# Performance work log

Measured on AMD Instinct MI355X. Metric: run time of the kernel, lower is better.

## Reference

```python
import jax, jax.numpy as jnp
import numpy as np

NUM_HEADING_BIN = 12
NUM_SIZE_CLUSTER = 8
DELTA_NORM_W = 0.01
CENTER_W = 0.5
B, N = 4096, 2048


def huber(err, delta=1.0):
    a = jnp.abs(err)
    q = jnp.minimum(a, delta)
    return jnp.mean(0.5 * q * q + delta * (a - q))


def box3d_corners(centers, headings, sizes):
    # centers (B,3), headings (B,), sizes (B,3) -> (B,8,3)
    l, w, h = sizes[:, 0:1], sizes[:, 1:2], sizes[:, 2:3]
    sx = jnp.asarray([1, 1, -1, -1, 1, 1, -1, -1], dtype=sizes.dtype)
    sy = jnp.asarray([1, -1, -1, 1, 1, -1, -1, 1], dtype=sizes.dtype)
    sz = jnp.asarray([1, 1, 1, 1, -1, -1, -1, -1], dtype=sizes.dtype)
    corners = jnp.stack([0.5 * l * sx, 0.5 * w * sy, 0.5 * h * sz], axis=1)  # (B,3,8)
    c, s = jnp.cos(headings), jnp.sin(headings)
    z, o = jnp.zeros_like(c), jnp.ones_like(c)
    R = jnp.stack([jnp.stack([c, -s, z], -1),
                   jnp.stack([s, c, z], -1),
                   jnp.stack([z, z, o], -1)], axis=1)  # (B,3,3)
    out = jnp.einsum('bij,bjk->bik', R, corners) + centers[:, :, None]
    return jnp.transpose(out, (0, 2, 1))  # (B,8,3)


def setup_inputs() -> dict:
    key = jax.random.key(0)
    ks = jax.random.split(key, 9)
    return {
        'mask_xyz_mean': jax.random.normal(ks[0], (B, 3), jnp.float32),
        'point_cloud': jax.random.normal(ks[1], (B, 3, N), jnp.float32),
        'x_delta': jax.random.normal(ks[2], (B, 3, N), jnp.float32),
        'center_label': jax.random.normal(ks[3], (B, 3), jnp.float32),
        'size_residual_label': jax.random.normal(ks[4], (B, 3), jnp.float32),
        'heading_residual_label': jax.random.normal(ks[5], (B,), jnp.float32),
        'mean_sizes': jax.random.uniform(ks[6], (NUM_SIZE_CLUSTER, 3), jnp.float32, 0.5, 2.5),
        'size_class_label': jax.random.randint(ks[7], (B,), 0, NUM_SIZE_CLUSTER, jnp.int32),
        'heading_class_label': jax.random.randint(ks[8], (B,), 0, NUM_HEADING_BIN, jnp.int32),
    }


def reference(mask_xyz_mean, point_cloud, x_delta, center_label,
              size_residual_label, heading_residual_label, mean_sizes,
              size_class_label, heading_class_label):
    eps = 0.0  # faithful: original has no eps
    # center loss
    center_dist = jnp.linalg.norm(mask_xyz_mean - center_label, axis=1)
    center_loss = CENTER_W * huber(center_dist)

    # label assembly (onehot-sum == gather)
    size_label = mean_sizes[size_class_label] + size_residual_label  # (B,3)
    bin_centers = jnp.arange(0, np.pi, np.pi / NUM_HEADING_BIN, dtype=jnp.float32)
    heading_label = heading_residual_label + bin_centers[heading_class_label]  # (B,)

    corners_3d_gt = box3d_corners(center_label, heading_label, size_label)
    corners_2d_gt = corners_3d_gt[:, 4:8, :2]  # (B,4,2)

    v = center_label[:, :2]  # (B,2)
    p_dir = jnp.stack([-v[:, 1], v[:, 0]], axis=1)
    p_dir = p_dir / jnp.linalg.norm(p_dir, axis=1, keepdims=True)  # (B,2)

    pp_label = jnp.einsum('bkc,bc->bk', corners_2d_gt, p_dir)  # (B,4)
    py_max, py_min = jnp.max(pp_label, axis=1), jnp.min(pp_label, axis=1)
    std_y_label = (py_max - py_min) / 4
    mean_y_label = (py_max + py_min) / 2

    v_norm = jnp.linalg.norm(v, axis=1, keepdims=True)  # (B,1)
    proj_label = jnp.einsum('bkc,bc->bk', corners_2d_gt, v) / v_norm  # (B,4)
    p_max, p_min = jnp.max(proj_label, axis=1), jnp.min(proj_label, axis=1)
    std_label = (p_max - p_min) / 4
    mean_label = (p_max + p_min) / 2

    pc_xy = jnp.transpose(point_cloud, (0, 2, 1))[:, :, :2]  # (B,N,2)

    pp_pc = jnp.einsum('bnc,bc->bn', pc_xy, p_dir)  # (B,N)
    std_y_pc = jnp.std(pp_pc, axis=1, ddof=1)
    mean_y_pc = jnp.mean(pp_pc, axis=1)
    y_std_loss = huber(jnp.abs(std_y_label - std_y_pc))
    y_mean_loss = huber(jnp.abs(mean_y_label - mean_y_pc))

    proj_pc = jnp.einsum('bnc,bc->bn', pc_xy, v) / v_norm  # (B,N)
    std_pc = jnp.std(proj_pc, axis=1, ddof=1)
    mean_pc = jnp.mean(proj_pc, axis=1)
    x_std_loss = huber(jnp.abs(std_label - std_pc))
    x_mean_loss = huber(jnp.abs(mean_label - mean_pc))

    delta_norm = jnp.sqrt(jnp.sum(x_delta * x_delta, axis=(1, 2)))
    delta_norm_loss = DELTA_NORM_W * huber(delta_norm)

    total = center_loss + x_std_loss + x_mean_loss + delta_norm_loss + y_mean_loss + y_std_loss
    return 0.4 * total
```

## Files before the change

### kernel.cpp

```cpp
#include <hip/hip_runtime.h>
#include <math.h>

#define B_SZ 4096
#define N_PTS 2048
#define BLOCK 256

__device__ __forceinline__ float huber1(float a) {
    float q = fminf(a, 1.0f);
    return 0.5f * q * q + (a - q);
}

__global__ __launch_bounds__(BLOCK) void loss_stage1(
    const float* __restrict__ point_cloud,
    const float* __restrict__ x_delta,
    const float* __restrict__ center_label,
    float4* __restrict__ ws_pc,
    float*  __restrict__ ws_d)
{
    const int tid  = threadIdx.x;
    const int wave = tid >> 6;
    const int lane = tid & 63;
    const int g    = lane >> 4;
    const int il   = lane & 15;

    if (blockIdx.x < 256) {
        const int quad = blockIdx.x * 4 + wave;
        const int e    = quad * 4 + g;

        const float cx = center_label[e * 3 + 0];
        const float cy = center_label[e * 3 + 1];
        const float vn = sqrtf(cx * cx + cy * cy);
        const float pdx = -cy / vn;
        const float pdy =  cx / vn;

        const float4* px = (const float4*)(point_cloud + (size_t)e * 3 * N_PTS);
        const float4* py = px + (N_PTS / 4);

        float s_pp = 0.f, s_pp2 = 0.f, s_t = 0.f, s_t2 = 0.f;

        #pragma unroll 4
        for (int k = 0; k < N_PTS / 4 / 16; ++k) {
            const float4 x4 = px[il + k * 16];
            const float4 y4 = py[il + k * 16];
            {
                const float pp = x4.x * pdx + y4.x * pdy;
                const float t  = x4.x * cx  + y4.x * cy;
                s_pp += pp; s_pp2 += pp * pp; s_t += t; s_t2 += t * t;
            }
            {
                const float pp = x4.y * pdx + y4.y * pdy;
                const float t  = x4.y * cx  + y4.y * cy;
                s_pp += pp; s_pp2 += pp * pp; s_t += t; s_t2 += t * t;
            }
            {
                const float pp = x4.z * pdx + y4.z * pdy;
                const float t  = x4.z * cx  + y4.z * cy;
                s_pp += pp; s_pp2 += pp * pp; s_t += t; s_t2 += t * t;
            }
            {
                const float pp = x4.w * pdx + y4.w * pdy;
                const float t  = x4.w * cx  + y4.w * cy;
                s_pp += pp; s_pp2 += pp * pp; s_t += t; s_t2 += t * t;
            }
        }

        #pragma unroll
        for (int off = 8; off > 0; off >>= 1) {
            s_pp  += __shfl_down(s_pp,  off, 64);
            s_pp2 += __shfl_down(s_pp2, off, 64);
            s_t   += __shfl_down(s_t,   off, 64);
            s_t2  += __shfl_down(s_t2,  off, 64);
        }
        if (il == 0) ws_pc[e] = make_float4(s_pp, s_pp2, s_t, s_t2);
    } else {
        const int quad = (blockIdx.x - 256) * 4 + wave;
        const int e    = quad * 4 + g;

        const float4* pd = (const float4*)(x_delta + (size_t)e * 3 * N_PTS);

        float a0 = 0.f, a1 = 0.f, a2 = 0.f, a3 = 0.f;
        #pragma unroll 8
        for (int k = 0; k < 3 * N_PTS / 4 / 16; ++k) {
            const float4 d = pd[il + k * 16];
            a0 += d.x * d.x;
            a1 += d.y * d.y;
            a2 += d.z * d.z;
            a3 += d.w * d.w;
        }
        float s = (a0 + a1) + (a2 + a3);

        #pragma unroll
        for (int off = 8; off > 0; off >>= 1)
            s += __shfl_down(s, off, 64);
        if (il == 0) ws_d[e] = s;
    }
}

__global__ __launch_bounds__(BLOCK) void loss_stage2(
    const float4* __restrict__ ws_pc,
    const float*  __restrict__ ws_d,
    const float* __restrict__ mask_xyz_mean,
    const float* __restrict__ center_label,
    const float* __restrict__ size_residual,
    const float* __restrict__ heading_residual,
    const float* __restrict__ mean_sizes,
    const int*   __restrict__ size_class,
    const int*   __restrict__ heading_class,
    float* __restrict__ ws_p)
{
    const int tid = threadIdx.x;
    const int b   = blockIdx.x * BLOCK + tid;

    const float4 pcs = ws_pc[b];
    const float s_pp = pcs.x, s_pp2 = pcs.y, s_t = pcs.z, s_t2 = pcs.w;
    const float s_d2 = ws_d[b];

    const float cx = center_label[b * 3 + 0];
    const float cy = center_label[b * 3 + 1];
    const float cz = center_label[b * 3 + 2];
    const float vnorm2 = cx * cx + cy * cy;
    const float vnorm  = sqrtf(vnorm2);
    const float pdx = -cy / vnorm;
    const float pdy =  cx / vnorm;

    const float mx = mask_xyz_mean[b * 3 + 0];
    const float my = mask_xyz_mean[b * 3 + 1];
    const float mz = mask_xyz_mean[b * 3 + 2];
    const float dxc = mx - cx, dyc = my - cy, dzc = mz - cz;
    const float center_dist = sqrtf(dxc * dxc + dyc * dyc + dzc * dzc);

    const int sc = size_class[b];
    const float l  = mean_sizes[sc * 3 + 0] + size_residual[b * 3 + 0];
    const float w_ = mean_sizes[sc * 3 + 1] + size_residual[b * 3 + 1];

    const float theta = heading_residual[b] +
                        (float)heading_class[b] * (float)(M_PI / 12.0);
    const float c = cosf(theta);
    const float s = sinf(theta);
    const float hl = 0.5f * l, hw = 0.5f * w_;

    float X[4], Y[4];
    X[0] =  c * hl - s * hw + cx;  Y[0] =  s * hl + c * hw + cy;
    X[1] =  c * hl + s * hw + cx;  Y[1] =  s * hl - c * hw + cy;
    X[2] = -c * hl + s * hw + cx;  Y[2] = -s * hl - c * hw + cy;
    X[3] = -c * hl - s * hw + cx;  Y[3] = -s * hl + c * hw + cy;

    float ppmax = -INFINITY, ppmin = INFINITY;
    float pmax  = -INFINITY, pmin  = INFINITY;
    #pragma unroll
    for (int k = 0; k < 4; ++k) {
        const float pp = X[k] * pdx + Y[k] * pdy;
        const float pj = (X[k] * cx + Y[k] * cy) / vnorm;
        ppmax = fmaxf(ppmax, pp); ppmin = fminf(ppmin, pp);
        pmax  = fmaxf(pmax,  pj); pmin  = fminf(pmin,  pj);
    }
    const float std_y_label  = (ppmax - ppmin) * 0.25f;
    const float mean_y_label = (ppmax + ppmin) * 0.5f;
    const float std_label    = (pmax - pmin) * 0.25f;
    const float mean_label   = (pmax + pmin) * 0.5f;

    const float invN   = 1.0f / (float)N_PTS;
    const float invNm1 = 1.0f / (float)(N_PTS - 1);

    const float mean_y_pc = s_pp * invN;
    const float var_y = (s_pp2 - s_pp * s_pp * invN) * invNm1;
    const float std_y_pc = sqrtf(fmaxf(var_y, 0.0f));

    const float mean_pc = (s_t * invN) / vnorm;
    const float var_x = ((s_t2 - s_t * s_t * invN) * invNm1) / vnorm2;
    const float std_pc = sqrtf(fmaxf(var_x, 0.0f));

    const float delta_norm = sqrtf(s_d2);

    float total =
          0.5f  * huber1(center_dist)
        +         huber1(fabsf(std_label  - std_pc))
        +         huber1(fabsf(mean_label - mean_pc))
        + 0.01f * huber1(delta_norm)
        +         huber1(fabsf(mean_y_label - mean_y_pc))
        +         huber1(fabsf(std_y_label  - std_y_pc));

    #pragma unroll
    for (int off = 32; off > 0; off >>= 1)
        total += __shfl_down(total, off, 64);

    __shared__ float red[BLOCK / 64];
    const int wave = tid >> 6;
    const int lane = tid & 63;
    if (lane == 0) red[wave] = total;
    __syncthreads();
    if (tid == 0) {
        #pragma unroll
        for (int w = 1; w < BLOCK / 64; ++w) total += red[w];
        ws_p[blockIdx.x] = total;
    }
}

__global__ void loss_stage3(const float* __restrict__ ws_p, float* __restrict__ out)
{
    const int lane = threadIdx.x;
    float s = (lane < B_SZ / BLOCK) ? ws_p[lane] : 0.0f;
    #pragma unroll
    for (int off = 32; off > 0; off >>= 1)
        s += __shfl_down(s, off, 64);
    if (lane == 0) out[0] = s * (0.4f / (float)B_SZ);
}

extern "C" void kernel_launch(void* const* d_in, const int* in_sizes, int n_in,
                              void* d_out, int out_size, void* d_ws, size_t ws_size,
                              hipStream_t stream) {
    const float* mask_xyz_mean    = (const float*)d_in[0];
    const float* point_cloud      = (const float*)d_in[1];
    const float* x_delta          = (const float*)d_in[2];
    const float* center_label     = (const float*)d_in[3];
    const float* size_residual    = (const float*)d_in[4];
    const float* heading_residual = (const float*)d_in[5];
    const float* mean_sizes       = (const float*)d_in[6];
    const int*   size_class       = (const int*)d_in[7];
    const int*   heading_class    = (const int*)d_in[8];
    float* out = (float*)d_out;

    float4* ws_pc = (float4*)d_ws;
    float*  ws_d  = (float*)d_ws + B_SZ * 4;
    float*  ws_p  = ws_d + B_SZ;

    loss_stage1<<<512, BLOCK, 0, stream>>>(
        point_cloud, x_delta, center_label, ws_pc, ws_d);
    loss_stage2<<<B_SZ / BLOCK, BLOCK, 0, stream>>>(
        ws_pc, ws_d, mask_xyz_mean, center_label, size_residual,
        heading_residual, mean_sizes, size_class, heading_class, ws_p);
    loss_stage3<<<1, 64, 0, stream>>>(ws_p, out);
}
```

Measured before the change: 227.7 us.

## Assign one wave per sample and split x_delta reduction into quarter-sample waves

Stage 1 now gives each point-cloud sample a full 64-lane wave instead of a 16-lane group, and splits each x_delta sample across four waves that each load six float4s with no loop. The grid grows from 512 to 5120 blocks. Stage 2 sums the four partial squared norms per sample. The aim is more memory-level parallelism and better latency hiding on a bandwidth-bound streaming reduction, at the cost of more blocks, more partial results and a slightly larger workspace.

```diff
diff --git a/kernel.cpp b/kernel.cpp
--- a/kernel.cpp
+++ b/kernel.cpp
@@ -15,17 +15,14 @@
     const float* __restrict__ x_delta,
     const float* __restrict__ center_label,
     float4* __restrict__ ws_pc,
-    float*  __restrict__ ws_d)
+    float*  __restrict__ ws_dq)
 {
     const int tid  = threadIdx.x;
     const int wave = tid >> 6;
     const int lane = tid & 63;
-    const int g    = lane >> 4;
-    const int il   = lane & 15;
-
-    if (blockIdx.x < 256) {
-        const int quad = blockIdx.x * 4 + wave;
-        const int e    = quad * 4 + g;
+
+    if (blockIdx.x < 1024) {
+        const int e = blockIdx.x * 4 + wave;
 
         const float cx = center_label[e * 3 + 0];
         const float cy = center_label[e * 3 + 1];
@@ -39,9 +36,9 @@
         float s_pp = 0.f, s_pp2 = 0.f, s_t = 0.f, s_t2 = 0.f;
 
         #pragma unroll 4
-        for (int k = 0; k < N_PTS / 4 / 16; ++k) {
-            const float4 x4 = px[il + k * 16];
-            const float4 y4 = py[il + k * 16];
+        for (int k = 0; k < N_PTS / 4 / 64; ++k) {
+            const float4 x4 = px[lane + k * 64];
+            const float4 y4 = py[lane + k * 64];
             {
                 const float pp = x4.x * pdx + y4.x * pdy;
                 const float t  = x4.x * cx  + y4.x * cy;
@@ -65,40 +62,46 @@
         }
 
         #pragma unroll
-        for (int off = 8; off > 0; off >>= 1) {
+        for (int off = 32; off > 0; off >>= 1) {
             s_pp  += __shfl_down(s_pp,  off, 64);
             s_pp2 += __shfl_down(s_pp2, off, 64);
             s_t   += __shfl_down(s_t,   off, 64);
             s_t2  += __shfl_down(s_t2,  off, 64);
         }
-        if (il == 0) ws_pc[e] = make_float4(s_pp, s_pp2, s_t, s_t2);
+        if (lane == 0) ws_pc[e] = make_float4(s_pp, s_pp2, s_t, s_t2);
     } else {
-        const int quad = (blockIdx.x - 256) * 4 + wave;
-        const int e    = quad * 4 + g;
-
-        const float4* pd = (const float4*)(x_delta + (size_t)e * 3 * N_PTS);
-
-        float a0 = 0.f, a1 = 0.f, a2 = 0.f, a3 = 0.f;
-        #pragma unroll 8
-        for (int k = 0; k < 3 * N_PTS / 4 / 16; ++k) {
-            const float4 d = pd[il + k * 16];
-            a0 += d.x * d.x;
-            a1 += d.y * d.y;
-            a2 += d.z * d.z;
-            a3 += d.w * d.w;
-        }
-        float s = (a0 + a1) + (a2 + a3);
+        const int w = (blockIdx.x - 1024) * 4 + wave;
+        const int s_idx = w >> 2;
+        const int q     = w & 3;
+
+        const float4* pd = (const float4*)x_delta +
+                           (size_t)s_idx * 1536 + q * 384;
+
+        float4 d0 = pd[lane];
+        float4 d1 = pd[lane + 64];
+        float4 d2 = pd[lane + 128];
+        float4 d3 = pd[lane + 192];
+        float4 d4 = pd[lane + 256];
+        float4 d5 = pd[lane + 320];
+
+        float a0 = d0.x * d0.x + d0.y * d0.y + d0.z * d0.z + d0.w * d0.w;
+        float a1 = d1.x * d1.x + d1.y * d1.y + d1.z * d1.z + d1.w * d1.w;
+        float a2 = d2.x * d2.x + d2.y * d2.y + d2.z * d2.z + d2.w * d2.w;
+        float a3 = d3.x * d3.x + d3.y * d3.y + d3.z * d3.z + d3.w * d3.w;
+        float a4 = d4.x * d4.x + d4.y * d4.y + d4.z * d4.z + d4.w * d4.w;
+        float a5 = d5.x * d5.x + d5.y * d5.y + d5.z * d5.z + d5.w * d5.w;
+        float s = ((a0 + a1) + (a2 + a3)) + (a4 + a5);
 
         #pragma unroll
-        for (int off = 8; off > 0; off >>= 1)
+        for (int off = 32; off > 0; off >>= 1)
             s += __shfl_down(s, off, 64);
-        if (il == 0) ws_d[e] = s;
+        if (lane == 0) ws_dq[w] = s;
     }
 }
 
 __global__ __launch_bounds__(BLOCK) void loss_stage2(
     const float4* __restrict__ ws_pc,
-    const float*  __restrict__ ws_d,
+    const float4* __restrict__ ws_dq4,
     const float* __restrict__ mask_xyz_mean,
     const float* __restrict__ center_label,
     const float* __restrict__ size_residual,
@@ -113,7 +116,8 @@
 
     const float4 pcs = ws_pc[b];
     const float s_pp = pcs.x, s_pp2 = pcs.y, s_t = pcs.z, s_t2 = pcs.w;
-    const float s_d2 = ws_d[b];
+    const float4 dq = ws_dq4[b];
+    const float s_d2 = (dq.x + dq.y) + (dq.z + dq.w);
 
     const float cx = center_label[b * 3 + 0];
     const float cy = center_label[b * 3 + 1];
@@ -221,13 +225,13 @@
     float* out = (float*)d_out;
 
     float4* ws_pc = (float4*)d_ws;
-    float*  ws_d  = (float*)d_ws + B_SZ * 4;
-    float*  ws_p  = ws_d + B_SZ;
-
-    loss_stage1<<<512, BLOCK, 0, stream>>>(
-        point_cloud, x_delta, center_label, ws_pc, ws_d);
+    float*  ws_dq = (float*)d_ws + B_SZ * 4;
+    float*  ws_p  = ws_dq + B_SZ * 4;
+
+    loss_stage1<<<5120, BLOCK, 0, stream>>>(
+        point_cloud, x_delta, center_label, ws_pc, ws_dq);
     loss_stage2<<<B_SZ / BLOCK, BLOCK, 0, stream>>>(
-        ws_pc, ws_d, mask_xyz_mean, center_label, size_residual,
+        ws_pc, (const float4*)ws_dq, mask_xyz_mean, center_label, size_residual,
         heading_residual, mean_sizes, size_class, heading_class, ws_p);
     loss_stage3<<<1, 64, 0, stream>>>(ws_p, out);
 }
```

New measurement: 222.8 us. 1.02x faster.
